# Kernel tuning notes

Hardware: AMD Instinct MI355X
Metric: run time of the kernel (lower is better)

The kernel has to match this reference:

```python
import jax, jax.numpy as jnp
import numpy as np

B, N, DIM, H, DH = 8, 1024, 512, 8, 64
INNER = H * DH
SCALE = DH ** -0.5


def setup_inputs() -> dict:
    key = jax.random.key(0)
    ks = jax.random.split(key, 9)
    s = 0.02
    return {
        "x": jax.random.normal(ks[0], (B, N, DIM), jnp.float32),
        "lidar": jax.random.normal(ks[1], (B, N, INNER), jnp.float32),
        "w_qkv": jax.random.normal(ks[2], (3 * INNER, DIM), jnp.float32) * s,
        "w_merge": jax.random.normal(ks[3], (DH, DH), jnp.float32) * s,
        "b_merge": jnp.zeros((DH,), jnp.float32),
        "w_out": jax.random.normal(ks[4], (DIM, INNER), jnp.float32) * s,
        "b_out": jnp.zeros((DIM,), jnp.float32),
        "conv_w": jax.random.normal(ks[5], (2,), jnp.float32) * 0.5,
        "conv_b": jnp.zeros((), jnp.float32),
    }


def _split_heads(t):  # [b, n, h*d] -> [b, h, n, d]
    b, n, _ = t.shape
    return t.reshape(b, n, H, DH).transpose(0, 2, 1, 3)


def reference(x, lidar, w_qkv, w_merge, b_merge, w_out, b_out, conv_w, conv_b):
    b, n, _ = x.shape
    qkv = x @ w_qkv.T  # [b, n, 3*inner]
    q, k, v = jnp.split(qkv, 3, axis=-1)
    q, k, v = _split_heads(q), _split_heads(k), _split_heads(v)
    lid = _split_heads(lidar)

    dots = jnp.einsum('bhid,bhjd->bhij', q, k) * SCALE
    lidar_sim = jnp.einsum('bhid,bhjd->bhij', lid, lid) * SCALE
    lidar_sim = jax.nn.softmax(lidar_sim, axis=-1)

    # 1x1 conv over 2 channels == learned linear blend of the two score maps
    mid = conv_w[0] * dots + conv_w[1] * lidar_sim + conv_b
    attn = jax.nn.softmax(mid, axis=-1)

    out = jnp.einsum('bhij,bhjd->bhid', attn, v)
    out = out @ w_merge.T + b_merge                  # per-head linear_merge
    out = out.transpose(0, 2, 1, 3).reshape(b, n, INNER)  # b h n d -> b n (h d)
    out = out @ w_out.T + b_out                      # to_out (dropout = identity)
    return (out, lidar)
```

## Files before the change

kernel.cpp:

```cpp
#include <hip/hip_runtime.h>
#include <hip/hip_bf16.h>

#define B_      8
#define N_      1024
#define DIM_    512
#define H_      8
#define DH_     64
#define INNER_  512
#define SCALE_  0.125f
#define LOG2E_  1.4426950408889634f

typedef __attribute__((ext_vector_type(8))) __bf16         bf16x8;
typedef __attribute__((ext_vector_type(8))) unsigned short ushort8;
typedef __attribute__((ext_vector_type(4))) float          f32x4;

union FragCast { ushort8 u; bf16x8 b; };
union FragU32  { unsigned int u[4]; bf16x8 b; };

__device__ inline bf16x8 ld_frag(const unsigned short* p) {
    FragCast f; f.u = *(const ushort8*)p; return f.b;
}

__device__ inline f32x4 mfma16(bf16x8 a, bf16x8 b, f32x4 c) {
    return __builtin_amdgcn_mfma_f32_16x16x32_bf16(a, b, c, 0, 0, 0);
}

__device__ inline float fexp2(float x) { return __builtin_amdgcn_exp2f(x); }

__device__ inline unsigned short f2bf(float x) {
    unsigned int u = __float_as_uint(x);
    unsigned int lsb = (u >> 16) & 1u;
    u += 0x7fffu + lsb;
    return (unsigned short)(u >> 16);
}

__device__ inline unsigned int pack_bf2(float hi, float lo) {
    return __builtin_amdgcn_perm(__float_as_uint(hi), __float_as_uint(lo), 0x07060302u);
}

__device__ inline void gl_lds(const unsigned short* g, unsigned short* l) {
    __builtin_amdgcn_global_load_lds(
        (const __attribute__((address_space(1))) unsigned int*)g,
        (__attribute__((address_space(3))) unsigned int*)l, 16, 0, 0);
}

#define BARF() do { asm volatile("" ::: "memory"); \
                    __builtin_amdgcn_s_barrier();  \
                    asm volatile("" ::: "memory"); } while (0)
#define WAITV(n) asm volatile("s_waitcnt vmcnt(" #n ")" ::: "memory")

#define KEEP8(x) do { FragU32 _k; _k.b = (x); \
    asm volatile("" :: "v"(_k.u[0]), "v"(_k.u[1]), "v"(_k.u[2]), "v"(_k.u[3])); } while (0)

__global__ __launch_bounds__(256) void k_convert(
    const float* __restrict__ x, const float* __restrict__ lidar,
    const float* __restrict__ wqkv, const float* __restrict__ wmerge,
    const float* __restrict__ wout,
    unsigned short* __restrict__ x_bf, unsigned short* __restrict__ lid_bf,
    float* __restrict__ out_lidar,
    unsigned short* __restrict__ wqkv_bf, unsigned short* __restrict__ wm_bf,
    unsigned short* __restrict__ wout_bf)
{
    const int bx = blockIdx.x, tid = threadIdx.x;
    const float* src; unsigned short* dst; bool isLid = false; long base;
    if (bx < 1024)      { src = x;      dst = x_bf;    base = (long)bx * 1024; }
    else if (bx < 2048) { src = lidar;  dst = lid_bf;  base = (long)(bx - 1024) * 1024; isLid = true; }
    else if (bx < 2240) { src = wqkv;   dst = wqkv_bf; base = (long)(bx - 2048) * 1024; }
    else if (bx < 2304) { src = wout;   dst = wout_bf; base = (long)(bx - 2240) * 1024; }
    else                { src = wmerge; dst = wm_bf;   base = 0; }
    for (int k = 0; k < 4; k++) {
        long j = base + k * 256 + tid;
        float4 v = ((const float4*)src)[j];
        ushort4 o;
        o.x = f2bf(v.x); o.y = f2bf(v.y); o.z = f2bf(v.z); o.w = f2bf(v.w);
        ((ushort4*)dst)[j] = o;
        if (isLid) ((float4*)out_lidar)[j] = v;
    }
}

__global__ __launch_bounds__(256) void k_gemm_qkv(
    const unsigned short* __restrict__ A, const unsigned short* __restrict__ Bm,
    unsigned short* __restrict__ C, unsigned short* __restrict__ vt,
    int M, int Nd, int K)
{
    __shared__ unsigned short sMem[128 * 136];
    unsigned short* sA = sMem;
    unsigned short* sB = sMem + 128 * 64;
    const int tid  = threadIdx.x;
    const int lane = tid & 63, wave = tid >> 6;
    const int q = lane >> 4, l15 = lane & 15, l7 = l15 & 7;
    const int xq0 = (q ^ l7) << 3, xq4 = ((q + 4) ^ l7) << 3;
    const int m0 = blockIdx.x * 128, n0 = blockIdx.y * 128;
    const int wm = (wave >> 1) * 64, wn = (wave & 1) * 64;
    f32x4 acc[4][4] = {};

    for (int k0 = 0; k0 < K; k0 += 64) {
        __syncthreads();
        for (int i = 0; i < 4; i++) {
            int c = i * 256 + tid;
            int row = c >> 3;
            int gcol = ((c & 7) ^ (row & 7)) << 3;
            gl_lds(&A[(long)(m0 + row) * K + k0 + gcol], &sA[c * 8]);
            gl_lds(&Bm[(long)(n0 + row) * K + k0 + gcol], &sB[c * 8]);
        }
        __syncthreads();
        for (int kk = 0; kk < 2; kk++) {
            const int xx = kk ? xq4 : xq0;
            bf16x8 af[4], bfr[4];
            for (int i = 0; i < 4; i++)
                af[i]  = ld_frag(&sA[(wm + i * 16 + l15) * 64 + xx]);
            for (int i = 0; i < 4; i++)
                bfr[i] = ld_frag(&sB[(wn + i * 16 + l15) * 64 + xx]);
            for (int mi = 0; mi < 4; mi++)
                for (int ni = 0; ni < 4; ni++)
                    acc[mi][ni] = mfma16(af[mi], bfr[ni], acc[mi][ni]);
        }
    }
    if (n0 < 1024) {
        for (int mi = 0; mi < 4; mi++)
            for (int ni = 0; ni < 4; ni++)
                for (int r = 0; r < 4; r++) {
                    int row = m0 + wm + mi * 16 + q * 4 + r;
                    int col = n0 + wn + ni * 16 + l15;
                    C[(long)row * Nd + col] = f2bf(acc[mi][ni][r]);
                }
    } else {
        __syncthreads();
        for (int mi = 0; mi < 4; mi++) {
            int t0 = wm + mi * 16 + q * 4;
            for (int ni = 0; ni < 4; ni++) {
                int f = wn + ni * 16 + l15;
                ushort4 o4;
                o4.x = f2bf(acc[mi][ni][0]); o4.y = f2bf(acc[mi][ni][1]);
                o4.z = f2bf(acc[mi][ni][2]); o4.w = f2bf(acc[mi][ni][3]);
                *(ushort4*)&sMem[f * 136 + t0] = o4;
            }
        }
        __syncthreads();
        const long fb = (long)(n0 - 1024) * (B_ * N_) + m0;
        for (int i = 0; i < 8; i++) {
            int g = i * 256 + tid;
            int f = g >> 4, grp = g & 15;
            int base = (grp >> 2) * 32 + (grp & 3) * 4;
            ushort4 a4 = *(const ushort4*)&sMem[f * 136 + base];
            ushort4 b4 = *(const ushort4*)&sMem[f * 136 + base + 16];
            ushort8 o8 = {a4.x, a4.y, a4.z, a4.w, b4.x, b4.y, b4.z, b4.w};
            *(ushort8*)&vt[fb + (long)f * (B_ * N_) + grp * 8] = o8;
        }
    }
}

__global__ __launch_bounds__(256) void k_gemm_out(
    const unsigned short* __restrict__ A, const unsigned short* __restrict__ Bm,
    const float* __restrict__ bias, float* __restrict__ C, int M, int Nd, int K)
{
    __shared__ unsigned short sA[128 * 64];
    __shared__ unsigned short sB[64 * 64];
    const int tid  = threadIdx.x;
    const int lane = tid & 63, wave = tid >> 6;
    const int q = lane >> 4, l15 = lane & 15, l7 = l15 & 7;
    const int xq0 = (q ^ l7) << 3, xq4 = ((q + 4) ^ l7) << 3;
    const int m0 = blockIdx.x * 128, n0 = blockIdx.y * 64;
    const int wm = (wave >> 1) * 64, wn = (wave & 1) * 32;
    f32x4 acc[4][2] = {};

    for (int k0 = 0; k0 < K; k0 += 64) {
        __syncthreads();
        for (int i = 0; i < 4; i++) {
            int c = i * 256 + tid;
            int row = c >> 3;
            int gcol = ((c & 7) ^ (row & 7)) << 3;
            gl_lds(&A[(long)(m0 + row) * K + k0 + gcol], &sA[c * 8]);
            if (i < 2)
                gl_lds(&Bm[(long)(n0 + row) * K + k0 + gcol], &sB[c * 8]);
        }
        __syncthreads();
        for (int kk = 0; kk < 2; kk++) {
            const int xx = kk ? xq4 : xq0;
            bf16x8 af[4], bfr[2];
            for (int i = 0; i < 4; i++)
                af[i]  = ld_frag(&sA[(wm + i * 16 + l15) * 64 + xx]);
            for (int i = 0; i < 2; i++)
                bfr[i] = ld_frag(&sB[(wn + i * 16 + l15) * 64 + xx]);
            for (int mi = 0; mi < 4; mi++)
                for (int ni = 0; ni < 2; ni++)
                    acc[mi][ni] = mfma16(af[mi], bfr[ni], acc[mi][ni]);
        }
    }
    for (int mi = 0; mi < 4; mi++)
        for (int ni = 0; ni < 2; ni++)
            for (int r = 0; r < 4; r++) {
                int row = m0 + wm + mi * 16 + q * 4 + r;
                int col = n0 + wn + ni * 16 + l15;
                C[(long)row * Nd + col] = acc[mi][ni][r] + bias[col];
            }
}


template <int SB>
__device__ __forceinline__ void comp1(const unsigned short* smem, int a0, int a4,
                                      const bf16x8* lfq, float sc, float& rsl)
{
#pragma unroll
    for (int ns = 0; ns < 8; ns++) {
        f32x4 cv = {0.f, 0.f, 0.f, 0.f};
        cv = mfma16(ld_frag(&smem[SB + ns * 1024 + a0]), lfq[0], cv);
        cv = mfma16(ld_frag(&smem[SB + ns * 1024 + a4]), lfq[1], cv);
#pragma unroll
        for (int r = 0; r < 4; r++) rsl += fexp2(cv[r] * sc);
    }
}

template <int KB>
__device__ __forceinline__ void comp2(const unsigned short* smem, int a0, int a4,
                                      const bf16x8* qf, const bf16x8* lfq,
                                      float k0c, float k2c, float k1, float sc,
                                      float& rs, f32x4* o)
{
#pragma unroll
    for (int ns2 = 0; ns2 < 2; ns2++) {
        FragU32 fa;
#pragma unroll
        for (int h2 = 0; h2 < 2; h2++) {
            const int ns = ns2 * 2 + h2;
            f32x4 a = {0.f, 0.f, 0.f, 0.f};
            a = mfma16(ld_frag(&smem[KB + ns * 1024 + a0]), qf[0], a);
            a = mfma16(ld_frag(&smem[KB + ns * 1024 + a4]), qf[1], a);
            f32x4 cv = {0.f, 0.f, 0.f, 0.f};
            cv = mfma16(ld_frag(&smem[KB + 4096 + ns * 1024 + a0]), lfq[0], cv);
            cv = mfma16(ld_frag(&smem[KB + 4096 + ns * 1024 + a4]), lfq[1], cv);
            float pv[4];
#pragma unroll
            for (int r = 0; r < 4; r++) {
                float els = fexp2(cv[r] * sc);
                float t = fmaf(k0c, a[r], k2c);
                t = fmaf(k1, els, t);
                pv[r] = fexp2(t);
                rs += pv[r];
            }
            fa.u[h2 * 2 + 0] = pack_bf2(pv[1], pv[0]);
            fa.u[h2 * 2 + 1] = pack_bf2(pv[3], pv[2]);
        }
        const int av = ns2 ? a4 : a0;
#pragma unroll
        for (int dt = 0; dt < 4; dt++)
            o[dt] = mfma16(fa.b, ld_frag(&smem[KB + 8192 + dt * 1024 + av]), o[dt]);
    }
}

__global__ __launch_bounds__(512) void k_flash(
    const unsigned short* __restrict__ qkv_bf, const unsigned short* __restrict__ lid_bf,
    const unsigned short* __restrict__ vt,
    const unsigned short* __restrict__ wm_bf, const float* __restrict__ b_merge,
    const float* __restrict__ conv_w, const float* __restrict__ conv_b,
    unsigned short* __restrict__ tmp_bf)
{
    __shared__ unsigned short smem[36864];
    __shared__ float sRS[8][16];

    const int tid = threadIdx.x, lane = tid & 63, wave = tid >> 6;
    const int q = lane >> 4, l15 = lane & 15, l7 = l15 & 7;
    const int xq0 = (q ^ l7) << 3, xq4 = ((q + 4) ^ l7) << 3;
    const int a0 = l15 * 64 + xq0, a4 = l15 * 64 + xq4;
    const int bh = blockIdx.x, ipair = blockIdx.y;
    const int b = bh >> 3, h = bh & 7;
    const int i0w = ipair * 128 + wave * 16;
    const long rowB = (long)b * N_;
    const int colh = h * DH_;
    const float k0c = conv_w[0] * SCALE_ * LOG2E_;
    const float k2c = conv_b[0] * LOG2E_;
    const float c1L = conv_w[1] * LOG2E_;
    const float sc = SCALE_ * LOG2E_;

    const int srow = tid >> 3;
    const int sgc  = ((tid & 7) ^ (srow & 7)) << 3;
    unsigned short* sd = &smem[tid * 8];
    const unsigned short* gK = &qkv_bf[(rowB + srow) * 1536 + 512 + colh + sgc];
    const unsigned short* gL = &lid_bf[(rowB + srow) * INNER_ + colh + sgc];
    const unsigned short* gV = &vt[(long)(colh + srow) * (B_ * N_) + rowB + sgc];
    const unsigned short* gL1a = &lid_bf[(rowB + srow) * INNER_ + colh + sgc];
    const unsigned short* gL1b = &lid_bf[(rowB + 64 + srow) * INNER_ + colh + sgc];

    bf16x8 qf[2], lfq[2];
#pragma unroll
    for (int ks = 0; ks < 2; ks++) {
        qf[ks]  = ld_frag(&qkv_bf[(rowB + i0w + l15) * 1536 + colh + ks * 32 + q * 8]);
        lfq[ks] = ld_frag(&lid_bf[(rowB + i0w + l15) * INNER_ + colh + ks * 32 + q * 8]);
    }
    KEEP8(qf[0]); KEEP8(qf[1]); KEEP8(lfq[0]); KEEP8(lfq[1]);
    WAITV(0);

#define ISS1(off) do { gl_lds(gL1a, sd + (off)); gl_lds(gL1b, sd + (off) + 4096); \
                       gL1a += 128 * INNER_; gL1b += 128 * INNER_; } while (0)
#define ISS2(off) do { gl_lds(gK, sd + (off)); gl_lds(gL, sd + (off) + 4096); \
                       gl_lds(gV, sd + (off) + 8192); \
                       gK += 64 * 1536; gL += 64 * INNER_; gV += 64; } while (0)

    float rsl = 0.f;
    ISS1(0); ISS1(8192);
#pragma unroll
    for (int t = 0; t < 8; t++) {
        if (t < 7) { WAITV(2); } else { WAITV(0); }
        BARF();
        __builtin_amdgcn_s_setprio(1);
        if      (t % 3 == 0) comp1<0>    (smem, a0, a4, lfq, sc, rsl);
        else if (t % 3 == 1) comp1<8192> (smem, a0, a4, lfq, sc, rsl);
        else                 comp1<16384>(smem, a0, a4, lfq, sc, rsl);
        __builtin_amdgcn_s_setprio(0);
        if (t + 2 < 8) {
            if      ((t + 2) % 3 == 0) ISS1(0);
            else if ((t + 2) % 3 == 1) ISS1(8192);
            else                       ISS1(16384);
        }
    }

    BARF();
    ISS2(0); ISS2(12288);
    rsl += __shfl_xor(rsl, 16);
    rsl += __shfl_xor(rsl, 32);
    const float k1 = c1L / rsl;
    float rs = 0.f;
    f32x4 o[4] = {};

#pragma unroll
    for (int t = 0; t < 16; t++) {
        if (t < 15) { WAITV(3); } else { WAITV(0); }
        BARF();
        __builtin_amdgcn_s_setprio(1);
        if      (t % 3 == 0) comp2<0>    (smem, a0, a4, qf, lfq, k0c, k2c, k1, sc, rs, o);
        else if (t % 3 == 1) comp2<12288>(smem, a0, a4, qf, lfq, k0c, k2c, k1, sc, rs, o);
        else                 comp2<24576>(smem, a0, a4, qf, lfq, k0c, k2c, k1, sc, rs, o);
        __builtin_amdgcn_s_setprio(0);
        if (t + 2 < 16) {
            if      ((t + 2) % 3 == 0) ISS2(0);
            else if ((t + 2) % 3 == 1) ISS2(12288);
            else                       ISS2(24576);
        }
    }
#undef ISS1
#undef ISS2
    BARF();

    rs += __shfl_xor(rs, 16);
    rs += __shfl_xor(rs, 32);
    if (q == 0) sRS[wave][l15] = rs;
    float invr[4];
    for (int r = 0; r < 4; r++) invr[r] = 1.f / sRS[wave][q * 4 + r];

    unsigned short* pO = &smem[wave * 16 * 72];
#pragma unroll
    for (int dt = 0; dt < 4; dt++)
        for (int r = 0; r < 4; r++)
            pO[(q * 4 + r) * 72 + dt * 16 + l15] = f2bf(o[dt][r] * invr[r]);

    f32x4 mo[4] = {};
#pragma unroll
    for (int ks = 0; ks < 2; ks++) {
        bf16x8 af = ld_frag(&pO[l15 * 72 + ks * 32 + q * 8]);
#pragma unroll
        for (int ns = 0; ns < 4; ns++) {
            bf16x8 wf = ld_frag(&wm_bf[(ns * 16 + l15) * 64 + ks * 32 + q * 8]);
            mo[ns] = mfma16(af, wf, mo[ns]);
        }
    }
#pragma unroll
    for (int ns = 0; ns < 4; ns++) {
        float bm = b_merge[ns * 16 + l15];
        for (int r = 0; r < 4; r++) {
            long row = rowB + i0w + q * 4 + r;
            tmp_bf[row * INNER_ + colh + ns * 16 + l15] = f2bf(mo[ns][r] + bm);
        }
    }
}

extern "C" void kernel_launch(void* const* d_in, const int* in_sizes, int n_in,
                              void* d_out, int out_size, void* d_ws, size_t ws_size,
                              hipStream_t stream) {
    const float* x       = (const float*)d_in[0];
    const float* lidar   = (const float*)d_in[1];
    const float* w_qkv   = (const float*)d_in[2];
    const float* w_merge = (const float*)d_in[3];
    const float* b_merge = (const float*)d_in[4];
    const float* w_out   = (const float*)d_in[5];
    const float* b_out   = (const float*)d_in[6];
    const float* conv_w  = (const float*)d_in[7];
    const float* conv_b  = (const float*)d_in[8];

    float* out0      = (float*)d_out;
    float* out_lidar = out0 + (long)B_ * N_ * INNER_;

    size_t off = 0;
    auto carve = [&](size_t bytes) {
        void* p = (char*)d_ws + off;
        off += (bytes + 255) & ~(size_t)255;
        return p;
    };
    unsigned short* qkv_bf  = (unsigned short*)carve((size_t)B_ * N_ * 3 * INNER_ * 2);
    unsigned short* lid_bf  = (unsigned short*)carve((size_t)B_ * N_ * INNER_ * 2);
    unsigned short* x_bf    = (unsigned short*)carve((size_t)B_ * N_ * DIM_ * 2);
    unsigned short* wqkv_bf = (unsigned short*)carve((size_t)3 * INNER_ * DIM_ * 2);
    unsigned short* wout_bf = (unsigned short*)carve((size_t)DIM_ * INNER_ * 2);
    unsigned short* wm_bf   = (unsigned short*)carve((size_t)DH_ * DH_ * 2);
    unsigned short* tmp_bf  = (unsigned short*)carve((size_t)B_ * N_ * INNER_ * 2);
    unsigned short* vt_bf   = (unsigned short*)carve((size_t)INNER_ * B_ * N_ * 2);

    k_convert<<<2305, 256, 0, stream>>>(x, lidar, w_qkv, w_merge, w_out,
                                        x_bf, lid_bf, out_lidar,
                                        wqkv_bf, wm_bf, wout_bf);

    k_gemm_qkv<<<dim3(64, 12), 256, 0, stream>>>(
        x_bf, wqkv_bf, qkv_bf, vt_bf, B_ * N_, 3 * INNER_, DIM_);

    k_flash<<<dim3(64, 8), 512, 0, stream>>>(
        qkv_bf, lid_bf, vt_bf, wm_bf, b_merge, conv_w, conv_b, tmp_bf);

    k_gemm_out<<<dim3(64, 8), 256, 0, stream>>>(
        tmp_bf, wout_bf, b_out, out0, B_ * N_, DIM_, INNER_);
}
```

Baseline: 179.1 us.

## Move lidar and weight conversions into QKV GEMM launch to overlap

Splits the fp32-to-bf16 conversion kernel so it only converts x and w_qkv, which the QKV GEMM needs. The lidar copy/convert and the w_out and w_merge conversions move into extra blocks of the QKV GEMM launch, using a flattened 1D grid. Those blocks can run alongside the GEMM tiles, hiding memory-bound conversion work under compute-bound GEMM work and shortening the serial first kernel. The GEMM and conversion blocks now compete for CUs within one launch.

```diff
diff --git a/kernel.cpp b/kernel.cpp
--- a/kernel.cpp
+++ b/kernel.cpp
@@ -53,44 +53,56 @@
     asm volatile("" :: "v"(_k.u[0]), "v"(_k.u[1]), "v"(_k.u[2]), "v"(_k.u[3])); } while (0)
 
 __global__ __launch_bounds__(256) void k_convert(
-    const float* __restrict__ x, const float* __restrict__ lidar,
-    const float* __restrict__ wqkv, const float* __restrict__ wmerge,
-    const float* __restrict__ wout,
-    unsigned short* __restrict__ x_bf, unsigned short* __restrict__ lid_bf,
-    float* __restrict__ out_lidar,
-    unsigned short* __restrict__ wqkv_bf, unsigned short* __restrict__ wm_bf,
-    unsigned short* __restrict__ wout_bf)
+    const float* __restrict__ x, const float* __restrict__ wqkv,
+    unsigned short* __restrict__ x_bf, unsigned short* __restrict__ wqkv_bf)
 {
     const int bx = blockIdx.x, tid = threadIdx.x;
-    const float* src; unsigned short* dst; bool isLid = false; long base;
-    if (bx < 1024)      { src = x;      dst = x_bf;    base = (long)bx * 1024; }
-    else if (bx < 2048) { src = lidar;  dst = lid_bf;  base = (long)(bx - 1024) * 1024; isLid = true; }
-    else if (bx < 2240) { src = wqkv;   dst = wqkv_bf; base = (long)(bx - 2048) * 1024; }
-    else if (bx < 2304) { src = wout;   dst = wout_bf; base = (long)(bx - 2240) * 1024; }
-    else                { src = wmerge; dst = wm_bf;   base = 0; }
+    const float* src; unsigned short* dst; long base;
+    if (bx < 1024) { src = x;    dst = x_bf;    base = (long)bx * 1024; }
+    else           { src = wqkv; dst = wqkv_bf; base = (long)(bx - 1024) * 1024; }
     for (int k = 0; k < 4; k++) {
         long j = base + k * 256 + tid;
         float4 v = ((const float4*)src)[j];
         ushort4 o;
         o.x = f2bf(v.x); o.y = f2bf(v.y); o.z = f2bf(v.z); o.w = f2bf(v.w);
         ((ushort4*)dst)[j] = o;
-        if (isLid) ((float4*)out_lidar)[j] = v;
     }
 }
 
 __global__ __launch_bounds__(256) void k_gemm_qkv(
     const unsigned short* __restrict__ A, const unsigned short* __restrict__ Bm,
     unsigned short* __restrict__ C, unsigned short* __restrict__ vt,
-    int M, int Nd, int K)
+    const float* __restrict__ lidar, float* __restrict__ out_lidar,
+    unsigned short* __restrict__ lid_bf,
+    const float* __restrict__ wout, unsigned short* __restrict__ wout_bf,
+    const float* __restrict__ wmerge, unsigned short* __restrict__ wm_bf)
 {
     __shared__ unsigned short sMem[128 * 136];
+    const int bx = blockIdx.x, tid = threadIdx.x;
+
+    if (bx >= 768) {
+        const float* src; unsigned short* dst; bool isLid = false; long base;
+        if (bx < 1792)      { src = lidar;  dst = lid_bf;  base = (long)(bx - 768) * 1024; isLid = true; }
+        else if (bx < 1856) { src = wout;   dst = wout_bf; base = (long)(bx - 1792) * 1024; }
+        else                { src = wmerge; dst = wm_bf;   base = 0; }
+        for (int k = 0; k < 4; k++) {
+            long j = base + k * 256 + tid;
+            float4 v = ((const float4*)src)[j];
+            ushort4 o;
+            o.x = f2bf(v.x); o.y = f2bf(v.y); o.z = f2bf(v.z); o.w = f2bf(v.w);
+            ((ushort4*)dst)[j] = o;
+            if (isLid) ((float4*)out_lidar)[j] = v;
+        }
+        return;
+    }
+
     unsigned short* sA = sMem;
     unsigned short* sB = sMem + 128 * 64;
-    const int tid  = threadIdx.x;
+    const int K = DIM_, Nd = 3 * INNER_;
     const int lane = tid & 63, wave = tid >> 6;
     const int q = lane >> 4, l15 = lane & 15, l7 = l15 & 7;
     const int xq0 = (q ^ l7) << 3, xq4 = ((q + 4) ^ l7) << 3;
-    const int m0 = blockIdx.x * 128, n0 = blockIdx.y * 128;
+    const int m0 = (bx & 63) * 128, n0 = (bx >> 6) * 128;
     const int wm = (wave >> 1) * 64, wn = (wave & 1) * 64;
     f32x4 acc[4][4] = {};
 
@@ -404,12 +416,12 @@
     unsigned short* tmp_bf  = (unsigned short*)carve((size_t)B_ * N_ * INNER_ * 2);
     unsigned short* vt_bf   = (unsigned short*)carve((size_t)INNER_ * B_ * N_ * 2);
 
-    k_convert<<<2305, 256, 0, stream>>>(x, lidar, w_qkv, w_merge, w_out,
-                                        x_bf, lid_bf, out_lidar,
-                                        wqkv_bf, wm_bf, wout_bf);
-
-    k_gemm_qkv<<<dim3(64, 12), 256, 0, stream>>>(
-        x_bf, wqkv_bf, qkv_bf, vt_bf, B_ * N_, 3 * INNER_, DIM_);
+    k_convert<<<1216, 256, 0, stream>>>(x, w_qkv, x_bf, wqkv_bf);
+
+    k_gemm_qkv<<<1857, 256, 0, stream>>>(
+        x_bf, wqkv_bf, qkv_bf, vt_bf,
+        lidar, out_lidar, lid_bf,
+        w_out, wout_bf, w_merge, wm_bf);
 
     k_flash<<<dim3(64, 8), 512, 0, stream>>>(
         qkv_bf, lid_bf, vt_bf, wm_bf, b_merge, conv_w, conv_b, tmp_bf);
```

Result: no change. 182.2 us (+1.8%).

## Triple-buffer GEMM K-loop with async global-to-LDS prefetch and halve QKV tile width

Applied to the files above, without the earlier changes.

Both projection GEMMs now use a three-stage LDS ring. Async global-to-LDS loads for upcoming K-steps are issued two steps ahead and gated by vmcnt waits, replacing the load/sync/compute loop with its two barriers per step. The QKV GEMM tile shrinks from 128x128 to 128x64, doubling its grid to give more blocks, at the cost of less reuse of the A tile. LDS use grows to 72KB per block, which may limit occupancy.

```diff
diff --git a/kernel.cpp b/kernel.cpp
--- a/kernel.cpp
+++ b/kernel.cpp
@@ -78,72 +78,103 @@
     }
 }
 
+template <int KB>
+__device__ __forceinline__ void gemm_step(const unsigned short* smem,
+                                          int wm, int wn, int l15,
+                                          int xq0, int xq4, f32x4 acc[4][2])
+{
+#pragma unroll
+    for (int kk = 0; kk < 2; kk++) {
+        const int xx = kk ? xq4 : xq0;
+        bf16x8 af[4], bfr[2];
+#pragma unroll
+        for (int i = 0; i < 4; i++)
+            af[i]  = ld_frag(&smem[KB + (wm + i * 16 + l15) * 64 + xx]);
+#pragma unroll
+        for (int i = 0; i < 2; i++)
+            bfr[i] = ld_frag(&smem[KB + 8192 + (wn + i * 16 + l15) * 64 + xx]);
+#pragma unroll
+        for (int mi = 0; mi < 4; mi++)
+#pragma unroll
+            for (int ni = 0; ni < 2; ni++)
+                acc[mi][ni] = mfma16(af[mi], bfr[ni], acc[mi][ni]);
+    }
+}
+
 __global__ __launch_bounds__(256) void k_gemm_qkv(
     const unsigned short* __restrict__ A, const unsigned short* __restrict__ Bm,
-    unsigned short* __restrict__ C, unsigned short* __restrict__ vt,
-    int M, int Nd, int K)
-{
-    __shared__ unsigned short sMem[128 * 136];
-    unsigned short* sA = sMem;
-    unsigned short* sB = sMem + 128 * 64;
+    unsigned short* __restrict__ C, unsigned short* __restrict__ vt)
+{
+    __shared__ unsigned short smem[36864];
     const int tid  = threadIdx.x;
     const int lane = tid & 63, wave = tid >> 6;
     const int q = lane >> 4, l15 = lane & 15, l7 = l15 & 7;
     const int xq0 = (q ^ l7) << 3, xq4 = ((q + 4) ^ l7) << 3;
-    const int m0 = blockIdx.x * 128, n0 = blockIdx.y * 128;
-    const int wm = (wave >> 1) * 64, wn = (wave & 1) * 64;
-    f32x4 acc[4][4] = {};
-
-    for (int k0 = 0; k0 < K; k0 += 64) {
-        __syncthreads();
-        for (int i = 0; i < 4; i++) {
-            int c = i * 256 + tid;
-            int row = c >> 3;
-            int gcol = ((c & 7) ^ (row & 7)) << 3;
-            gl_lds(&A[(long)(m0 + row) * K + k0 + gcol], &sA[c * 8]);
-            gl_lds(&Bm[(long)(n0 + row) * K + k0 + gcol], &sB[c * 8]);
-        }
-        __syncthreads();
-        for (int kk = 0; kk < 2; kk++) {
-            const int xx = kk ? xq4 : xq0;
-            bf16x8 af[4], bfr[4];
-            for (int i = 0; i < 4; i++)
-                af[i]  = ld_frag(&sA[(wm + i * 16 + l15) * 64 + xx]);
-            for (int i = 0; i < 4; i++)
-                bfr[i] = ld_frag(&sB[(wn + i * 16 + l15) * 64 + xx]);
-            for (int mi = 0; mi < 4; mi++)
-                for (int ni = 0; ni < 4; ni++)
-                    acc[mi][ni] = mfma16(af[mi], bfr[ni], acc[mi][ni]);
-        }
-    }
+    const int m0 = blockIdx.x * 128, n0 = blockIdx.y * 64;
+    const int wm = (wave >> 1) * 64, wn = (wave & 1) * 32;
+    const int K = DIM_, Nd = 3 * INNER_;
+    f32x4 acc[4][2] = {};
+
+    const int r0  = tid >> 3;
+    const int gc  = ((tid & 7) ^ (r0 & 7)) << 3;
+    const unsigned short* gA0 = &A [(long)(m0 + r0      ) * K + gc];
+    const unsigned short* gA1 = &A [(long)(m0 + r0 +  32) * K + gc];
+    const unsigned short* gA2 = &A [(long)(m0 + r0 +  64) * K + gc];
+    const unsigned short* gA3 = &A [(long)(m0 + r0 +  96) * K + gc];
+    const unsigned short* gB0 = &Bm[(long)(n0 + r0      ) * K + gc];
+    const unsigned short* gB1 = &Bm[(long)(n0 + r0 +  32) * K + gc];
+    unsigned short* sd = &smem[tid * 8];
+
+#define ISSG(off) do { \
+    gl_lds(gA0, sd + (off));        gl_lds(gA1, sd + (off) + 2048);  \
+    gl_lds(gA2, sd + (off) + 4096); gl_lds(gA3, sd + (off) + 6144);  \
+    gl_lds(gB0, sd + (off) + 8192); gl_lds(gB1, sd + (off) + 10240); \
+    gA0 += 64; gA1 += 64; gA2 += 64; gA3 += 64; gB0 += 64; gB1 += 64; } while (0)
+
+    ISSG(0); ISSG(12288);
+#pragma unroll
+    for (int t = 0; t < 8; t++) {
+        if (t < 7) { WAITV(6); } else { WAITV(0); }
+        BARF();
+        if      (t % 3 == 0) gemm_step<0>    (smem, wm, wn, l15, xq0, xq4, acc);
+        else if (t % 3 == 1) gemm_step<12288>(smem, wm, wn, l15, xq0, xq4, acc);
+        else                 gemm_step<24576>(smem, wm, wn, l15, xq0, xq4, acc);
+        if (t + 2 < 8) {
+            if      ((t + 2) % 3 == 0) ISSG(0);
+            else if ((t + 2) % 3 == 1) ISSG(12288);
+            else                       ISSG(24576);
+        }
+    }
+#undef ISSG
+
     if (n0 < 1024) {
         for (int mi = 0; mi < 4; mi++)
-            for (int ni = 0; ni < 4; ni++)
+            for (int ni = 0; ni < 2; ni++)
                 for (int r = 0; r < 4; r++) {
                     int row = m0 + wm + mi * 16 + q * 4 + r;
                     int col = n0 + wn + ni * 16 + l15;
                     C[(long)row * Nd + col] = f2bf(acc[mi][ni][r]);
                 }
     } else {
-        __syncthreads();
+        BARF();
         for (int mi = 0; mi < 4; mi++) {
             int t0 = wm + mi * 16 + q * 4;
-            for (int ni = 0; ni < 4; ni++) {
+            for (int ni = 0; ni < 2; ni++) {
                 int f = wn + ni * 16 + l15;
                 ushort4 o4;
                 o4.x = f2bf(acc[mi][ni][0]); o4.y = f2bf(acc[mi][ni][1]);
                 o4.z = f2bf(acc[mi][ni][2]); o4.w = f2bf(acc[mi][ni][3]);
-                *(ushort4*)&sMem[f * 136 + t0] = o4;
+                *(ushort4*)&smem[f * 136 + t0] = o4;
             }
         }
-        __syncthreads();
+        BARF();
         const long fb = (long)(n0 - 1024) * (B_ * N_) + m0;
-        for (int i = 0; i < 8; i++) {
+        for (int i = 0; i < 4; i++) {
             int g = i * 256 + tid;
             int f = g >> 4, grp = g & 15;
             int base = (grp >> 2) * 32 + (grp & 3) * 4;
-            ushort4 a4 = *(const ushort4*)&sMem[f * 136 + base];
-            ushort4 b4 = *(const ushort4*)&sMem[f * 136 + base + 16];
+            ushort4 a4 = *(const ushort4*)&smem[f * 136 + base];
+            ushort4 b4 = *(const ushort4*)&smem[f * 136 + base + 16];
             ushort8 o8 = {a4.x, a4.y, a4.z, a4.w, b4.x, b4.y, b4.z, b4.w};
             *(ushort8*)&vt[fb + (long)f * (B_ * N_) + grp * 8] = o8;
         }
@@ -152,41 +183,50 @@
 
 __global__ __launch_bounds__(256) void k_gemm_out(
     const unsigned short* __restrict__ A, const unsigned short* __restrict__ Bm,
-    const float* __restrict__ bias, float* __restrict__ C, int M, int Nd, int K)
-{
-    __shared__ unsigned short sA[128 * 64];
-    __shared__ unsigned short sB[64 * 64];
+    const float* __restrict__ bias, float* __restrict__ C)
+{
+    __shared__ unsigned short smem[36864];
     const int tid  = threadIdx.x;
     const int lane = tid & 63, wave = tid >> 6;
     const int q = lane >> 4, l15 = lane & 15, l7 = l15 & 7;
     const int xq0 = (q ^ l7) << 3, xq4 = ((q + 4) ^ l7) << 3;
     const int m0 = blockIdx.x * 128, n0 = blockIdx.y * 64;
     const int wm = (wave >> 1) * 64, wn = (wave & 1) * 32;
+    const int K = INNER_, Nd = DIM_;
     f32x4 acc[4][2] = {};
 
-    for (int k0 = 0; k0 < K; k0 += 64) {
-        __syncthreads();
-        for (int i = 0; i < 4; i++) {
-            int c = i * 256 + tid;
-            int row = c >> 3;
-            int gcol = ((c & 7) ^ (row & 7)) << 3;
-            gl_lds(&A[(long)(m0 + row) * K + k0 + gcol], &sA[c * 8]);
-            if (i < 2)
-                gl_lds(&Bm[(long)(n0 + row) * K + k0 + gcol], &sB[c * 8]);
-        }
-        __syncthreads();
-        for (int kk = 0; kk < 2; kk++) {
-            const int xx = kk ? xq4 : xq0;
-            bf16x8 af[4], bfr[2];
-            for (int i = 0; i < 4; i++)
-                af[i]  = ld_frag(&sA[(wm + i * 16 + l15) * 64 + xx]);
-            for (int i = 0; i < 2; i++)
-                bfr[i] = ld_frag(&sB[(wn + i * 16 + l15) * 64 + xx]);
-            for (int mi = 0; mi < 4; mi++)
-                for (int ni = 0; ni < 2; ni++)
-                    acc[mi][ni] = mfma16(af[mi], bfr[ni], acc[mi][ni]);
-        }
-    }
+    const int r0  = tid >> 3;
+    const int gc  = ((tid & 7) ^ (r0 & 7)) << 3;
+    const unsigned short* gA0 = &A [(long)(m0 + r0      ) * K + gc];
+    const unsigned short* gA1 = &A [(long)(m0 + r0 +  32) * K + gc];
+    const unsigned short* gA2 = &A [(long)(m0 + r0 +  64) * K + gc];
+    const unsigned short* gA3 = &A [(long)(m0 + r0 +  96) * K + gc];
+    const unsigned short* gB0 = &Bm[(long)(n0 + r0      ) * K + gc];
+    const unsigned short* gB1 = &Bm[(long)(n0 + r0 +  32) * K + gc];
+    unsigned short* sd = &smem[tid * 8];
+
+#define ISSG(off) do { \
+    gl_lds(gA0, sd + (off));        gl_lds(gA1, sd + (off) + 2048);  \
+    gl_lds(gA2, sd + (off) + 4096); gl_lds(gA3, sd + (off) + 6144);  \
+    gl_lds(gB0, sd + (off) + 8192); gl_lds(gB1, sd + (off) + 10240); \
+    gA0 += 64; gA1 += 64; gA2 += 64; gA3 += 64; gB0 += 64; gB1 += 64; } while (0)
+
+    ISSG(0); ISSG(12288);
+#pragma unroll
+    for (int t = 0; t < 8; t++) {
+        if (t < 7) { WAITV(6); } else { WAITV(0); }
+        BARF();
+        if      (t % 3 == 0) gemm_step<0>    (smem, wm, wn, l15, xq0, xq4, acc);
+        else if (t % 3 == 1) gemm_step<12288>(smem, wm, wn, l15, xq0, xq4, acc);
+        else                 gemm_step<24576>(smem, wm, wn, l15, xq0, xq4, acc);
+        if (t + 2 < 8) {
+            if      ((t + 2) % 3 == 0) ISSG(0);
+            else if ((t + 2) % 3 == 1) ISSG(12288);
+            else                       ISSG(24576);
+        }
+    }
+#undef ISSG
+
     for (int mi = 0; mi < 4; mi++)
         for (int ni = 0; ni < 2; ni++)
             for (int r = 0; r < 4; r++) {
@@ -195,7 +235,6 @@
                 C[(long)row * Nd + col] = acc[mi][ni][r] + bias[col];
             }
 }
-
 
 template <int SB>
 __device__ __forceinline__ void comp1(const unsigned short* smem, int a0, int a4,
@@ -408,12 +447,12 @@
                                         x_bf, lid_bf, out_lidar,
                                         wqkv_bf, wm_bf, wout_bf);
 
-    k_gemm_qkv<<<dim3(64, 12), 256, 0, stream>>>(
-        x_bf, wqkv_bf, qkv_bf, vt_bf, B_ * N_, 3 * INNER_, DIM_);
+    k_gemm_qkv<<<dim3(64, 24), 256, 0, stream>>>(
+        x_bf, wqkv_bf, qkv_bf, vt_bf);
 
     k_flash<<<dim3(64, 8), 512, 0, stream>>>(
         qkv_bf, lid_bf, vt_bf, wm_bf, b_merge, conv_w, conv_b, tmp_bf);
 
     k_gemm_out<<<dim3(64, 8), 256, 0, stream>>>(
-        tmp_bf, wout_bf, b_out, out0, B_ * N_, DIM_, INNER_);
-}
+        tmp_bf, wout_bf, b_out, out0);
+}
```

Result: faster. 175.1 us (-2.2%).
